# Kernel optimization log

Hardware: AMD Instinct MI355X
Metric: run time of the kernel (lower is better)

The kernel has to match this reference:

```python
import jax, jax.numpy as jnp
import numpy as np

B, S, D, H = 8, 2048, 1024, 64

def setup_inputs() -> dict:
    key = jax.random.key(0)
    ks = jax.random.split(key, 7)
    scale = 0.02
    return {
        "x": jax.random.normal(ks[0], (B, S, D), dtype=jnp.float32),
        "Wq": jax.random.normal(ks[1], (D, H), dtype=jnp.float32) * scale,
        "bq": jax.random.normal(ks[2], (H,), dtype=jnp.float32) * scale,
        "Wk": jax.random.normal(ks[3], (D, H), dtype=jnp.float32) * scale,
        "bk": jax.random.normal(ks[4], (H,), dtype=jnp.float32) * scale,
        "Wv": jax.random.normal(ks[5], (D, H), dtype=jnp.float32) * scale,
        "bv": jax.random.normal(ks[6], (H,), dtype=jnp.float32) * scale,
    }

def reference(x, Wq, bq, Wk, bk, Wv, bv):
    # Single-head causal self-attention (dropout in eval mode -> identity).
    q = x @ Wq + bq            # [B,S,H]
    k = x @ Wk + bk            # [B,S,H]
    v = x @ Wv + bv            # [B,S,H]
    scores = jnp.einsum("bqh,bkh->bqk", q, k)  # [B,S,S]
    s = q.shape[1]
    causal = jnp.tril(jnp.ones((s, s), dtype=bool))
    # Original masks with -inf BEFORE scaling; -inf/scale == -inf, so equivalent.
    scores = jnp.where(causal, scores, -jnp.inf) / jnp.sqrt(jnp.float32(k.shape[-1]))
    attn = jax.nn.softmax(scores, axis=-1)
    return jnp.einsum("bqk,bkh->bqh", attn, v)
```

## Files before the change

### kernel.cpp

```cpp
#include <hip/hip_runtime.h>
#include <math.h>

#define BATCH 8
#define SEQ   2048
#define DIM   1024
#define HD    64
#define NROWS (BATCH * SEQ)
#define CHUNK 256
#define NCHUNK 8
#define QTILE 64
#define NQT   (SEQ / QTILE)
#define QSCALE 0.1803368801f

typedef __attribute__((ext_vector_type(8))) short bf16x8;
typedef __attribute__((ext_vector_type(4))) float f32x4;

__device__ __forceinline__ unsigned short f2bf(float f) {
    unsigned u = __float_as_uint(f);
    u = (u + 0x7FFFu + ((u >> 16) & 1u)) >> 16;
    return (unsigned short)u;
}
__device__ __forceinline__ unsigned short f2bf_hu(float f) {
    return (unsigned short)((__float_as_uint(f) + 0x8000u) >> 16);
}
__device__ __forceinline__ float fast_exp2(float x) {
#if __has_builtin(__builtin_amdgcn_exp2f)
    return __builtin_amdgcn_exp2f(x);
#else
    return exp2f(x);
#endif
}

__device__ __forceinline__ void gld_lds16(const void* g, void* l) {
    __builtin_amdgcn_global_load_lds(
        (const __attribute__((address_space(1))) void*)g,
        (__attribute__((address_space(3))) void*)l, 16, 0, 0);
}

__device__ __forceinline__ uint4 pack_bf16x8(float4 a, float4 b) {
    uint4 o;
    o.x = ((__float_as_uint(a.x) + 0x8000u) >> 16) | ((__float_as_uint(a.y) + 0x8000u) & 0xFFFF0000u);
    o.y = ((__float_as_uint(a.z) + 0x8000u) >> 16) | ((__float_as_uint(a.w) + 0x8000u) & 0xFFFF0000u);
    o.z = ((__float_as_uint(b.x) + 0x8000u) >> 16) | ((__float_as_uint(b.y) + 0x8000u) & 0xFFFF0000u);
    o.w = ((__float_as_uint(b.z) + 0x8000u) >> 16) | ((__float_as_uint(b.w) + 0x8000u) & 0xFFFF0000u);
    return o;
}

#define CFENCE() asm volatile("" ::: "memory")
#define RAW_BAR() do { CFENCE(); __builtin_amdgcn_s_barrier(); CFENCE(); } while (0)

__global__ __launch_bounds__(256)
void prep_w_kernel(const float* __restrict__ Wq, const float* __restrict__ Wk,
                   const float* __restrict__ Wv, unsigned short* __restrict__ Wt)
{
    const int mat = blockIdx.y;
    const float* __restrict__ W = (mat == 0) ? Wq : (mat == 1) ? Wk : Wv;
    const int k0 = blockIdx.x * 64;
    __shared__ float T[64][65];
    const int t = threadIdx.x;
    #pragma unroll
    for (int i = 0; i < 16; ++i) {
        const int idx = t + i * 256;
        T[idx >> 6][idx & 63] = W[(size_t)(k0 + (idx >> 6)) * HD + (idx & 63)];
    }
    __syncthreads();
    const int n = t >> 2;
    const int c = t & 3;
    union { unsigned short h[16]; uint4 v[2]; } buf;
    #pragma unroll
    for (int j = 0; j < 16; ++j) buf.h[j] = f2bf(T[c * 16 + j][n]);
    unsigned short* dst = Wt + ((size_t)mat * HD + n) * DIM + k0 + c * 16;
    *(uint4*)dst       = buf.v[0];
    *(uint4*)(dst + 8) = buf.v[1];
}

__global__ __launch_bounds__(768)
void qkv_mfma_kernel(const float* __restrict__ x,
                     const unsigned short* __restrict__ Wt,
                     const float* __restrict__ bq, const float* __restrict__ bk,
                     const float* __restrict__ bv,
                     unsigned short* __restrict__ Qg,
                     unsigned short* __restrict__ Kg,
                     unsigned short* __restrict__ Vtg)
{
    __shared__ unsigned short Xs[2][64][64];
    __shared__ unsigned short Ws[2][192][64];

    const int t    = threadIdx.x;
    const int lane = t & 63;
    const int w    = t >> 6;
    const int col  = lane & 15;
    const int quad = lane >> 4;
    const int mat  = w >> 2;
    const int wr   = w & 3;
    const int row0 = blockIdx.x * 64;

    const int r8  = lane >> 3;
    const int ch8 = lane & 7;
    const int wswz = (ch8 ^ r8) * 8;

    f32x4 acc[4];
    #pragma unroll
    for (int i = 0; i < 4; ++i) acc[i] = (f32x4){0.f, 0.f, 0.f, 0.f};

    const int xr  = t >> 3;
    const int xc0 = t & 7;
    const float* __restrict__ xrow = &x[(size_t)(row0 + xr) * DIM];

    auto stageW = [&](int it, int bb) {
        const int k0 = it * 64;
        #pragma unroll
        for (int ii = 0; ii < 2; ++ii) {
            const int rbase = w * 16 + ii * 8;
            gld_lds16(&Wt[(size_t)(rbase + r8) * DIM + k0 + wswz], &Ws[bb][rbase][0]);
        }
    };
    auto computeT = [&](int bb) {
        #pragma unroll
        for (int ks = 0; ks < 2; ++ks) {
            const int fswz = ((ks * 4 + quad) ^ (col & 7)) * 8;
            const bf16x8 a = *(const bf16x8*)&Xs[bb][wr * 16 + col][fswz];
            #pragma unroll
            for (int nt = 0; nt < 4; ++nt) {
                const bf16x8 b = *(const bf16x8*)&Ws[bb][mat * 64 + nt * 16 + col][fswz];
                acc[nt] = __builtin_amdgcn_mfma_f32_16x16x32_bf16(a, b, acc[nt], 0, 0, 0);
            }
        }
    };

    float4 xa, xb;
    stageW(0, 0);
    if (t < 512) {
        xa = *(const float4*)(xrow + xc0 * 8);
        xb = *(const float4*)(xrow + xc0 * 8 + 4);
    }
    asm volatile("s_waitcnt vmcnt(0)" ::: "memory");
    if (t < 512) {
        *(uint4*)&Xs[0][xr][(xc0 ^ (xr & 7)) * 8] = pack_bf16x8(xa, xb);
        xa = *(const float4*)(xrow + 64 + xc0 * 8);
        xb = *(const float4*)(xrow + 64 + xc0 * 8 + 4);
    }

    int buf = 0;
    for (int it = 0; it < 16; ++it) {
        RAW_BAR();
        if (it < 15) {
            stageW(it + 1, buf ^ 1);
            asm volatile("s_waitcnt vmcnt(2)" ::: "memory");
            if (t < 512) {
                *(uint4*)&Xs[buf ^ 1][xr][(xc0 ^ (xr & 7)) * 8] = pack_bf16x8(xa, xb);
                if (it < 14) {
                    const float* xp = xrow + (it + 2) * 64;
                    xa = *(const float4*)(xp + xc0 * 8);
                    xb = *(const float4*)(xp + xc0 * 8 + 4);
                }
            }
        } else {
            asm volatile("s_waitcnt vmcnt(0)" ::: "memory");
        }
        RAW_BAR();
        computeT(buf);
        buf ^= 1;
    }

    const int b    = row0 / SEQ;
    const int s0   = (row0 % SEQ) + wr * 16 + quad * 4;
    const int grow = row0 + wr * 16 + quad * 4;
    const float* __restrict__ bias = (mat == 0) ? bq : (mat == 1) ? bk : bv;
    const float oscale = (mat == 0) ? QSCALE : 1.0f;
    #pragma unroll
    for (int nt = 0; nt < 4; ++nt) {
        const int nn = nt * 16 + col;
        const float bvv = bias[nn];
        if (mat < 2) {
            unsigned short* __restrict__ o = (mat == 0) ? Qg : Kg;
            #pragma unroll
            for (int r = 0; r < 4; ++r)
                o[(size_t)(grow + r) * HD + nn] = f2bf((acc[nt][r] + bvv) * oscale);
        } else {
            const unsigned lo = (unsigned)f2bf(acc[nt][0] + bvv) | ((unsigned)f2bf(acc[nt][1] + bvv) << 16);
            const unsigned hi = (unsigned)f2bf(acc[nt][2] + bvv) | ((unsigned)f2bf(acc[nt][3] + bvv) << 16);
            *(uint2*)&Vtg[((size_t)b * HD + nn) * SEQ + s0] = make_uint2(lo, hi);
        }
    }
}

__global__ __launch_bounds__(256)
void attn_part_kernel(const unsigned short* __restrict__ Qg,
                      const unsigned short* __restrict__ Kg,
                      const unsigned short* __restrict__ Vtg,
                      unsigned short* __restrict__ Opart,
                      float* __restrict__ Lsum)
{
    const int b = blockIdx.x;
    int y = blockIdx.y, c = 0;
    while (y >= 32 - 4 * c) { y -= 32 - 4 * c; ++c; }
    const int qt = y + 4 * c;

    __shared__ unsigned short Ks[64][64];
    __shared__ unsigned short Vs[64][64];
    __shared__ unsigned short Ps[4][16][76];

    const int t    = threadIdx.x;
    const int w    = t >> 6;
    const int lane = t & 63;
    const int col  = lane & 15;
    const int quad = lane >> 4;
    const int q0w  = qt * QTILE + w * 16;
    const size_t gq = (size_t)b * SEQ + q0w;

    const bf16x8 aq0 = *(const bf16x8*)&Qg[(gq + col) * HD + quad * 8];
    const bf16x8 aq1 = *(const bf16x8*)&Qg[(gq + col) * HD + 32 + quad * 8];

    f32x4 oacc[4];
    #pragma unroll
    for (int n = 0; n < 4; ++n) oacc[n] = (f32x4){0.f, 0.f, 0.f, 0.f};
    float lpart[4] = {0.f, 0.f, 0.f, 0.f};

    const int kbeg   = c * CHUNK;
    const int kend   = min((c + 1) * CHUNK, (qt + 1) * QTILE);
    const int ntiles = (kend - kbeg + 63) >> 6;

    const int r8 = lane >> 3, ch = lane & 7;
    const int swzr = (ch ^ r8) * 8;
    const unsigned short* kgb = Kg  + (size_t)b * SEQ * HD;
    const unsigned short* vgb = Vtg + (size_t)b * HD * SEQ;

    for (int it = 0; it < ntiles; ++it) {
        const int j0 = kbeg + it * 64;
        __syncthreads();
        #pragma unroll
        for (int ii = 0; ii < 2; ++ii) {
            const int rb = w * 16 + ii * 8;
            gld_lds16(&kgb[(size_t)(j0 + rb + r8) * HD + swzr], &Ks[rb][0]);
            gld_lds16(&vgb[(size_t)(rb + r8) * SEQ + j0 + swzr], &Vs[rb][0]);
        }
        __syncthreads();

        if (j0 <= q0w + 15) {
            f32x4 scv[4];
            #pragma unroll
            for (int nt = 0; nt < 4; ++nt) {
                const int sw0 = (quad ^ (col & 7)) * 8;
                const int sw1 = ((4 + quad) ^ (col & 7)) * 8;
                const bf16x8 bk0 = *(const bf16x8*)&Ks[nt * 16 + col][sw0];
                const bf16x8 bk1 = *(const bf16x8*)&Ks[nt * 16 + col][sw1];
                f32x4 s = __builtin_amdgcn_mfma_f32_16x16x32_bf16(aq0, bk0, (f32x4){0.f,0.f,0.f,0.f}, 0, 0, 0);
                s = __builtin_amdgcn_mfma_f32_16x16x32_bf16(aq1, bk1, s, 0, 0, 0);
                scv[nt] = s;
            }
            const bool needmask = (j0 + 63 > q0w);
            #pragma unroll
            for (int r = 0; r < 4; ++r) {
                const int row = q0w + quad * 4 + r;
                #pragma unroll
                for (int nt = 0; nt < 4; ++nt) {
                    float s = scv[nt][r];
                    if (needmask)
                        s = (j0 + nt * 16 + col <= row) ? s : -INFINITY;
                    const float p = fast_exp2(s);
                    lpart[r] += p;
                    Ps[w][quad * 4 + r][nt * 16 + col] = f2bf_hu(p);
                }
            }
            #pragma unroll
            for (int ks = 0; ks < 2; ++ks) {
                const bf16x8 ap = *(const bf16x8*)&Ps[w][col][ks * 32 + quad * 8];
                const int fswz = ((ks * 4 + quad) ^ (col & 7)) * 8;
                #pragma unroll
                for (int n = 0; n < 4; ++n) {
                    const bf16x8 bv2 = *(const bf16x8*)&Vs[n * 16 + col][fswz];
                    oacc[n] = __builtin_amdgcn_mfma_f32_16x16x32_bf16(ap, bv2, oacc[n], 0, 0, 0);
                }
            }
        }
    }

    #pragma unroll
    for (int r = 0; r < 4; ++r) {
        #pragma unroll
        for (int off = 1; off < 16; off <<= 1)
            lpart[r] += __shfl_xor(lpart[r], off, 64);
    }

    const int blk = (b * NQT + qt) * NCHUNK + c;
    unsigned short* Ob = Opart + (size_t)blk * (QTILE * HD);
    #pragma unroll
    for (int n = 0; n < 4; ++n)
        #pragma unroll
        for (int r = 0; r < 4; ++r)
            Ob[(w * 16 + quad * 4 + r) * HD + n * 16 + col] = f2bf(oacc[n][r]);
    if (col == 0) {
        float* lb = Lsum + (size_t)blk * QTILE;
        #pragma unroll
        for (int r = 0; r < 4; ++r)
            lb[w * 16 + quad * 4 + r] = lpart[r];
    }
}

__global__ __launch_bounds__(256)
void combine_kernel(const unsigned short* __restrict__ Opart,
                    const float* __restrict__ Lsum,
                    float* __restrict__ out)
{
    const int gid = blockIdx.x * 256 + threadIdx.x;
    const int i   = gid >> 4;
    const int d4  = (gid & 15) * 4;
    const int b   = i >> 11;
    const int s   = i & 2047;
    const int qt  = s >> 6;
    const int r64 = s & 63;
    const int nc  = (s >> 8) + 1;
    const int blk0 = (b * NQT + qt) * NCHUNK;

    float L = 0.f;
    float a0 = 0.f, a1 = 0.f, a2 = 0.f, a3 = 0.f;
    for (int cc = 0; cc < nc; ++cc) {
        L += Lsum[(size_t)(blk0 + cc) * QTILE + r64];
        const uint2 u = *(const uint2*)(Opart + (size_t)(blk0 + cc) * (QTILE * HD) + r64 * HD + d4);
        a0 += __uint_as_float(u.x << 16);
        a1 += __uint_as_float(u.x & 0xFFFF0000u);
        a2 += __uint_as_float(u.y << 16);
        a3 += __uint_as_float(u.y & 0xFFFF0000u);
    }
    const float rL = 1.0f / L;
    float4 o; o.x = a0 * rL; o.y = a1 * rL; o.z = a2 * rL; o.w = a3 * rL;
    *(float4*)&out[(size_t)i * HD + d4] = o;
}

extern "C" void kernel_launch(void* const* d_in, const int* in_sizes, int n_in,
                              void* d_out, int out_size, void* d_ws, size_t ws_size,
                              hipStream_t stream) {
    const float* x  = (const float*)d_in[0];
    const float* Wq = (const float*)d_in[1];
    const float* bq = (const float*)d_in[2];
    const float* Wk = (const float*)d_in[3];
    const float* bk = (const float*)d_in[4];
    const float* Wv = (const float*)d_in[5];
    const float* bv = (const float*)d_in[6];
    float* out = (float*)d_out;

    unsigned short* Wt    = (unsigned short*)d_ws;
    unsigned short* Qg    = Wt + (size_t)3 * HD * DIM;
    unsigned short* Kg    = Qg + (size_t)NROWS * HD;
    unsigned short* Vtg   = Kg + (size_t)NROWS * HD;
    unsigned short* Opart = Vtg + (size_t)BATCH * HD * SEQ;
    float* Lsum = (float*)(Opart + (size_t)BATCH * NQT * NCHUNK * QTILE * HD);

    prep_w_kernel<<<dim3(16, 3), 256, 0, stream>>>(Wq, Wk, Wv, Wt);
    qkv_mfma_kernel<<<dim3(NROWS / 64), 768, 0, stream>>>(x, Wt, bq, bk, bv, Qg, Kg, Vtg);
    attn_part_kernel<<<dim3(8, 144), 256, 0, stream>>>(Qg, Kg, Vtg, Opart, Lsum);
    combine_kernel<<<dim3(NROWS * 16 / 256), 256, 0, stream>>>(Opart, Lsum, out);
}
```

Baseline: 138.9 us.

## Double-buffer K/V tiles and enlarge query tiles and key chunks in attention

Each attention block now covers 128 queries with 8 waves, and key chunks are 512 wide, so the launch grid shrinks from 144 to 40 blocks per batch. K/V tiles are prefetched into a second LDS buffer while the current tile is computed, with raw barriers and explicit vmcnt waits replacing the two syncthreads per tile. The combine kernel's indexing is updated for the new tile and chunk sizes. The aim is to hide global-load latency and reduce duplicate K/V traffic, but the smaller grid and coarser causal load balance may reduce parallelism. The vmcnt(2) wait also assumes a specific count of outstanding loads per thread.

```diff
diff --git a/kernel.cpp b/kernel.cpp
--- a/kernel.cpp
+++ b/kernel.cpp
@@ -6,9 +6,9 @@
 #define DIM   1024
 #define HD    64
 #define NROWS (BATCH * SEQ)
-#define CHUNK 256
-#define NCHUNK 8
-#define QTILE 64
+#define CHUNK 512
+#define NCHUNK 4
+#define QTILE 128
 #define NQT   (SEQ / QTILE)
 #define QSCALE 0.1803368801f
 
@@ -185,7 +185,7 @@
     }
 }
 
-__global__ __launch_bounds__(256)
+__global__ __launch_bounds__(512)
 void attn_part_kernel(const unsigned short* __restrict__ Qg,
                       const unsigned short* __restrict__ Kg,
                       const unsigned short* __restrict__ Vtg,
@@ -194,12 +194,12 @@
 {
     const int b = blockIdx.x;
     int y = blockIdx.y, c = 0;
-    while (y >= 32 - 4 * c) { y -= 32 - 4 * c; ++c; }
+    while (y >= NQT - 4 * c) { y -= NQT - 4 * c; ++c; }
     const int qt = y + 4 * c;
 
-    __shared__ unsigned short Ks[64][64];
-    __shared__ unsigned short Vs[64][64];
-    __shared__ unsigned short Ps[4][16][76];
+    __shared__ unsigned short Ks[2][64][64];
+    __shared__ unsigned short Vs[2][64][64];
+    __shared__ unsigned short Ps[8][16][76];
 
     const int t    = threadIdx.x;
     const int w    = t >> 6;
@@ -226,16 +226,26 @@
     const unsigned short* kgb = Kg  + (size_t)b * SEQ * HD;
     const unsigned short* vgb = Vtg + (size_t)b * HD * SEQ;
 
+    auto stageKV = [&](int it, int bb) {
+        const int j0 = kbeg + it * 64;
+        const int rb = w * 8;
+        gld_lds16(&kgb[(size_t)(j0 + rb + r8) * HD + swzr], &Ks[bb][rb][0]);
+        gld_lds16(&vgb[(size_t)(rb + r8) * SEQ + j0 + swzr], &Vs[bb][rb][0]);
+    };
+
+    stageKV(0, 0);
+
+    int bufb = 0;
     for (int it = 0; it < ntiles; ++it) {
+        RAW_BAR();
+        if (it + 1 < ntiles) {
+            stageKV(it + 1, bufb ^ 1);
+            asm volatile("s_waitcnt vmcnt(2)" ::: "memory");
+        } else {
+            asm volatile("s_waitcnt vmcnt(0)" ::: "memory");
+        }
+        RAW_BAR();
         const int j0 = kbeg + it * 64;
-        __syncthreads();
-        #pragma unroll
-        for (int ii = 0; ii < 2; ++ii) {
-            const int rb = w * 16 + ii * 8;
-            gld_lds16(&kgb[(size_t)(j0 + rb + r8) * HD + swzr], &Ks[rb][0]);
-            gld_lds16(&vgb[(size_t)(rb + r8) * SEQ + j0 + swzr], &Vs[rb][0]);
-        }
-        __syncthreads();
 
         if (j0 <= q0w + 15) {
             f32x4 scv[4];
@@ -243,8 +253,8 @@
             for (int nt = 0; nt < 4; ++nt) {
                 const int sw0 = (quad ^ (col & 7)) * 8;
                 const int sw1 = ((4 + quad) ^ (col & 7)) * 8;
-                const bf16x8 bk0 = *(const bf16x8*)&Ks[nt * 16 + col][sw0];
-                const bf16x8 bk1 = *(const bf16x8*)&Ks[nt * 16 + col][sw1];
+                const bf16x8 bk0 = *(const bf16x8*)&Ks[bufb][nt * 16 + col][sw0];
+                const bf16x8 bk1 = *(const bf16x8*)&Ks[bufb][nt * 16 + col][sw1];
                 f32x4 s = __builtin_amdgcn_mfma_f32_16x16x32_bf16(aq0, bk0, (f32x4){0.f,0.f,0.f,0.f}, 0, 0, 0);
                 s = __builtin_amdgcn_mfma_f32_16x16x32_bf16(aq1, bk1, s, 0, 0, 0);
                 scv[nt] = s;
@@ -269,11 +279,12 @@
                 const int fswz = ((ks * 4 + quad) ^ (col & 7)) * 8;
                 #pragma unroll
                 for (int n = 0; n < 4; ++n) {
-                    const bf16x8 bv2 = *(const bf16x8*)&Vs[n * 16 + col][fswz];
+                    const bf16x8 bv2 = *(const bf16x8*)&Vs[bufb][n * 16 + col][fswz];
                     oacc[n] = __builtin_amdgcn_mfma_f32_16x16x32_bf16(ap, bv2, oacc[n], 0, 0, 0);
                 }
             }
         }
+        bufb ^= 1;
     }
 
     #pragma unroll
@@ -291,10 +302,10 @@
         for (int r = 0; r < 4; ++r)
             Ob[(w * 16 + quad * 4 + r) * HD + n * 16 + col] = f2bf(oacc[n][r]);
     if (col == 0) {
-        float* lb = Lsum + (size_t)blk * QTILE;
+        float* lb = Lsum + (size_t)blk * QTILE + w * 16;
         #pragma unroll
         for (int r = 0; r < 4; ++r)
-            lb[w * 16 + quad * 4 + r] = lpart[r];
+            lb[quad * 4 + r] = lpart[r];
     }
 }
 
@@ -308,16 +319,16 @@
     const int d4  = (gid & 15) * 4;
     const int b   = i >> 11;
     const int s   = i & 2047;
-    const int qt  = s >> 6;
-    const int r64 = s & 63;
-    const int nc  = (s >> 8) + 1;
+    const int qt  = s >> 7;
+    const int r   = s & 127;
+    const int nc  = (s >> 9) + 1;
     const int blk0 = (b * NQT + qt) * NCHUNK;
 
     float L = 0.f;
     float a0 = 0.f, a1 = 0.f, a2 = 0.f, a3 = 0.f;
     for (int cc = 0; cc < nc; ++cc) {
-        L += Lsum[(size_t)(blk0 + cc) * QTILE + r64];
-        const uint2 u = *(const uint2*)(Opart + (size_t)(blk0 + cc) * (QTILE * HD) + r64 * HD + d4);
+        L += Lsum[(size_t)(blk0 + cc) * QTILE + r];
+        const uint2 u = *(const uint2*)(Opart + (size_t)(blk0 + cc) * (QTILE * HD) + r * HD + d4);
         a0 += __uint_as_float(u.x << 16);
         a1 += __uint_as_float(u.x & 0xFFFF0000u);
         a2 += __uint_as_float(u.y << 16);
@@ -349,6 +360,6 @@
 
     prep_w_kernel<<<dim3(16, 3), 256, 0, stream>>>(Wq, Wk, Wv, Wt);
     qkv_mfma_kernel<<<dim3(NROWS / 64), 768, 0, stream>>>(x, Wt, bq, bk, bv, Qg, Kg, Vtg);
-    attn_part_kernel<<<dim3(8, 144), 256, 0, stream>>>(Qg, Kg, Vtg, Opart, Lsum);
+    attn_part_kernel<<<dim3(8, 40), 512, 0, stream>>>(Qg, Kg, Vtg, Opart, Lsum);
     combine_kernel<<<dim3(NROWS * 16 / 256), 256, 0, stream>>>(Opart, Lsum, out);
 }
```

Measured after the change: 138.2 us. Within noise of the previous version (-0.5%).
